# Optimization experiments

Measured on AMD Instinct MI355X. Metric: run time of the kernel, lower is better.

The kernel has to match this reference:

```python
import jax, jax.numpy as jnp
import numpy as np

B, LTMS, TTS, C_IN, F, H = 64, 16, 256, 128, 256, 256


def setup_inputs() -> dict:
    key = jax.random.key(0)
    ks = jax.random.split(key, 6)
    s = 0.05  # small init keeps relu-GRU numerically tame
    return {
        "x": jax.random.normal(ks[0], (B, LTMS * TTS, C_IN), dtype=jnp.float32),
        "conv_w": jax.random.normal(ks[1], (1, C_IN, F), dtype=jnp.float32) * s,
        "conv_b": jnp.zeros((F,), dtype=jnp.float32),
        "attn_w": jax.random.normal(ks[2], (TTS, TTS), dtype=jnp.float32) * s,
        "attn_b": jnp.zeros((TTS,), dtype=jnp.float32),
        "gru_w": jax.random.normal(ks[3], (F, 3 * H), dtype=jnp.float32) * s,
        "gru_u": jax.random.normal(ks[4], (H, 3 * H), dtype=jnp.float32) * s,
        "gru_b": jnp.zeros((2, 3 * H), dtype=jnp.float32),
    }


def _forward(x, conv_w, conv_b, attn_w, attn_b, gru_w, gru_u, gru_b):
    b = x.shape[0]
    # [B, LTMS*TTS, C] -> [B*LTMS, TTS, C]; segments are independent, so the
    # original per-segment Python loop vectorizes into the leading batch dim.
    xs = x.reshape(b * LTMS, TTS, C_IN)
    # Conv1D kernel_size=1 == pointwise GEMM, then ReLU (dropout=0 at inference)
    conv = jax.nn.relu(jnp.einsum('ntc,cf->ntf', xs, conv_w[0]) + conv_b)  # [N,T,F]
    # Attention: softmax(Dense) over time axis per filter, multiply back
    xt = conv.transpose(0, 2, 1)                                  # [N,F,T]
    probs = jax.nn.softmax(xt @ attn_w + attn_b, axis=-1)         # [N,F,T]
    x_att = conv * probs.transpose(0, 2, 1)                       # [N,T,F]
    # GRU (keras v2, reset_after=True), activation=relu, gate order z,r,h
    bi, br = gru_b[0], gru_b[1]
    gates_x = x_att @ gru_w + bi                                  # [N,T,3H]
    def step(h, gx):
        rec = h @ gru_u + br
        xz, xr, xh = jnp.split(gx, 3, axis=-1)
        rz, rr, rh = jnp.split(rec, 3, axis=-1)
        z = jax.nn.sigmoid(xz + rz)
        r = jax.nn.sigmoid(xr + rr)
        hh = jax.nn.relu(xh + r * rh)
        h_new = z * h + (1.0 - z) * hh
        return h_new, None
    h0 = jnp.zeros((b * LTMS, H), dtype=x.dtype)
    h_final, _ = jax.lax.scan(step, h0, gates_x.transpose(1, 0, 2))
    return h_final.reshape(b, LTMS, H)


def reference(x, conv_w, conv_b, attn_w, attn_b, gru_w, gru_u, gru_b):
    return _forward(x, conv_w, conv_b, attn_w, attn_b, gru_w, gru_u, gru_b)
```

## Files before the change

### kernel.cpp

```cpp
#include <hip/hip_runtime.h>
#include <stdint.h>

typedef unsigned short u16;
typedef __attribute__((ext_vector_type(8))) __bf16 bf16x8;
typedef __attribute__((ext_vector_type(4))) float f32x4;

#define TTS 256
#define NSEG 1024
#define TC 32

__device__ __forceinline__ u16 f2bf(float f) {
  union { float f; uint32_t u; } v; v.f = f;
  uint32_t r = v.u + 0x7fffu + ((v.u >> 16) & 1u);
  return (u16)(r >> 16);
}
__device__ __forceinline__ float bf2f(u16 h) {
  union { uint32_t u; float f; } v; v.u = ((uint32_t)h) << 16;
  return v.f;
}
__device__ __forceinline__ float sigm(float x) {
  return __builtin_amdgcn_rcpf(1.0f + __expf(-x));
}

__global__ void k_transp(const float* __restrict__ in, u16* __restrict__ out, int R, int C) {
  int i = blockIdx.x * blockDim.x + threadIdx.x;
  if (i < R * C) {
    int r = i / C, c = i % C;
    out[(size_t)c * R + r] = f2bf(in[i]);
  }
}

template <bool RELU, bool STORE_T, int AMODE>
__global__ __launch_bounds__(256) void k_gemm(
    const void* __restrict__ Av, const u16* __restrict__ Bt,
    const float* __restrict__ bias, u16* __restrict__ out, int K, int Nld, int t0) {
  __shared__ u16 ldsA[4096];
  __shared__ u16 ldsB[4096];
  const int tid  = threadIdx.x;
  const int w    = tid >> 6;
  const int lane = tid & 63;
  const int quad = lane >> 4;
  const int l16  = lane & 15;
  const int m0 = blockIdx.x * 128;
  const int n0 = blockIdx.y * 128;
  const int wm = w >> 1, wn = w & 1;
  const int srow = tid & 127, shalf = tid >> 7;

  f32x4 acc[4][4];
#pragma unroll
  for (int i = 0; i < 4; i++)
#pragma unroll
    for (int j = 0; j < 4; j++) acc[i][j] = f32x4{0.f, 0.f, 0.f, 0.f};

  for (int k0 = 0; k0 < K; k0 += 32) {
    ushort4 va[2][2]; bf16x8 vb[2];
#pragma unroll
    for (int q = 0; q < 2; q++) {
      int c = shalf * 2 + q;
      int kk = k0 + c * 8;
      if (AMODE == 0) {
        const float* Af = (const float*)Av;
        float4 f0 = *(const float4*)(Af + (size_t)(m0 + srow) * K + kk);
        float4 f1 = *(const float4*)(Af + (size_t)(m0 + srow) * K + kk + 4);
        va[q][0] = ushort4{f2bf(f0.x), f2bf(f0.y), f2bf(f0.z), f2bf(f0.w)};
        va[q][1] = ushort4{f2bf(f1.x), f2bf(f1.y), f2bf(f1.z), f2bf(f1.w)};
      } else {
        const u16* Ax = (const u16*)Av;
        int r = m0 + srow;
        const bf16x8 v = *(const bf16x8*)(Ax + (size_t)(r >> 5) * 65536 +
                          (size_t)(kk >> 6) * 16384 + (t0 + (r & 31)) * 64 + (kk & 63));
        va[q][0] = ((const ushort4*)&v)[0];
        va[q][1] = ((const ushort4*)&v)[1];
      }
      vb[q] = *(const bf16x8*)(Bt + (size_t)(n0 + srow) * K + kk);
    }
    __syncthreads();
#pragma unroll
    for (int q = 0; q < 2; q++) {
      int c = shalf * 2 + q;
      *(ushort4*)&ldsA[(c * 128 + srow) * 8]     = va[q][0];
      *(ushort4*)&ldsA[(c * 128 + srow) * 8 + 4] = va[q][1];
      *(bf16x8*)&ldsB[(c * 128 + srow) * 8] = vb[q];
    }
    __syncthreads();
    bf16x8 a[4], b[4];
#pragma unroll
    for (int i = 0; i < 4; i++)
      a[i] = *(const bf16x8*)&ldsA[(quad * 128 + wm * 64 + i * 16 + l16) * 8];
#pragma unroll
    for (int j = 0; j < 4; j++)
      b[j] = *(const bf16x8*)&ldsB[(quad * 128 + wn * 64 + j * 16 + l16) * 8];
#pragma unroll
    for (int i = 0; i < 4; i++)
#pragma unroll
      for (int j = 0; j < 4; j++)
        acc[i][j] = __builtin_amdgcn_mfma_f32_16x16x32_bf16(a[i], b[j], acc[i][j], 0, 0, 0);
  }

#pragma unroll
  for (int j = 0; j < 4; j++) {
    int col = n0 + wn * 64 + j * 16 + l16;
    float bv = bias[col];
#pragma unroll
    for (int i = 0; i < 4; i++) {
      int row0 = m0 + wm * 64 + i * 16 + quad * 4;
      if (STORE_T) {
        int nseg = row0 >> 8, tt0 = row0 & 255;
        ushort4 o;
        float v0 = acc[i][j][0] + bv, v1 = acc[i][j][1] + bv;
        float v2 = acc[i][j][2] + bv, v3 = acc[i][j][3] + bv;
        if (RELU) {
          v0 = fmaxf(v0, 0.f); v1 = fmaxf(v1, 0.f);
          v2 = fmaxf(v2, 0.f); v3 = fmaxf(v3, 0.f);
        }
        o.x = f2bf(v0); o.y = f2bf(v1); o.z = f2bf(v2); o.w = f2bf(v3);
        *(ushort4*)&out[(size_t)nseg * 65536 + (size_t)(col >> 6) * 16384 +
                        (col & 63) * 256 + tt0] = o;
      } else {
#pragma unroll
        for (int r = 0; r < 4; r++) {
          float v = acc[i][j][r] + bv;
          if (RELU) v = fmaxf(v, 0.f);
          out[(size_t)(row0 + r) * Nld + col] = f2bf(v);
        }
      }
    }
  }
}

__global__ __launch_bounds__(256) void k_attn(
    u16* xac,
    const u16* __restrict__ Wt,
    const float* __restrict__ attn_b) {
  __shared__ u16 ldsW[8192];
  __shared__ u16 ldsC[16384];
  __shared__ float redmax[4][64];
  __shared__ float redsum[4][64];
  const int tid  = threadIdx.x;
  const int w    = tid >> 6;
  const int lane = tid & 63;
  const int quad = lane >> 4;
  const int l16  = lane & 15;
  const int seg = blockIdx.x;
  const int c4  = blockIdx.y;
  u16* reg = xac + (size_t)seg * 65536 + (size_t)c4 * 16384;

  {
    const int f = tid & 63, g = tid >> 6;
#pragma unroll
    for (int u = 0; u < 8; u++) {
      int tch = g * 8 + u;
      *(bf16x8*)&ldsC[(tch * 64 + f) * 8] =
          *(const bf16x8*)(reg + (size_t)f * 256 + tch * 8);
    }
  }

  f32x4 acc[4][4];
#pragma unroll
  for (int i = 0; i < 4; i++)
#pragma unroll
    for (int j = 0; j < 4; j++) acc[i][j] = f32x4{0.f, 0.f, 0.f, 0.f};

  for (int s = 0; s < 8; s++) {
    int k0 = s * 32;
    bf16x8 vw[4];
#pragma unroll
    for (int c = 0; c < 4; c++)
      vw[c] = *(const bf16x8*)(Wt + (size_t)tid * 256 + k0 + c * 8);
    __syncthreads();
#pragma unroll
    for (int c = 0; c < 4; c++)
      *(bf16x8*)&ldsW[(c * 256 + tid) * 8] = vw[c];
    __syncthreads();
    bf16x8 a[4], b[4];
#pragma unroll
    for (int i = 0; i < 4; i++)
      a[i] = *(const bf16x8*)&ldsW[(quad * 256 + w * 64 + i * 16 + l16) * 8];
#pragma unroll
    for (int j = 0; j < 4; j++)
      b[j] = *(const bf16x8*)&ldsC[((s * 4 + quad) * 64 + j * 16 + l16) * 8];
#pragma unroll
    for (int i = 0; i < 4; i++)
#pragma unroll
      for (int j = 0; j < 4; j++)
        acc[i][j] = __builtin_amdgcn_mfma_f32_16x16x32_bf16(a[i], b[j], acc[i][j], 0, 0, 0);
  }

#pragma unroll
  for (int i = 0; i < 4; i++)
#pragma unroll
    for (int r = 0; r < 4; r++) {
      float ab = attn_b[w * 64 + i * 16 + quad * 4 + r];
#pragma unroll
      for (int j = 0; j < 4; j++) acc[i][j][r] += ab;
    }

  float lmax[4];
#pragma unroll
  for (int j = 0; j < 4; j++) {
    float m = -1e30f;
#pragma unroll
    for (int i = 0; i < 4; i++)
#pragma unroll
      for (int r = 0; r < 4; r++) m = fmaxf(m, acc[i][j][r]);
    m = fmaxf(m, __shfl_xor(m, 16));
    m = fmaxf(m, __shfl_xor(m, 32));
    lmax[j] = m;
  }
  __syncthreads();
  if (quad == 0) {
#pragma unroll
    for (int j = 0; j < 4; j++) redmax[w][j * 16 + l16] = lmax[j];
  }
  __syncthreads();
  float gmax[4];
#pragma unroll
  for (int j = 0; j < 4; j++) {
    int c = j * 16 + l16;
    gmax[j] = fmaxf(fmaxf(redmax[0][c], redmax[1][c]), fmaxf(redmax[2][c], redmax[3][c]));
  }
  float lsum[4];
#pragma unroll
  for (int j = 0; j < 4; j++) {
    float sacc = 0.f;
#pragma unroll
    for (int i = 0; i < 4; i++)
#pragma unroll
      for (int r = 0; r < 4; r++) {
        float e = __expf(acc[i][j][r] - gmax[j]);
        acc[i][j][r] = e;
        sacc += e;
      }
    sacc += __shfl_xor(sacc, 16);
    sacc += __shfl_xor(sacc, 32);
    lsum[j] = sacc;
  }
  if (quad == 0) {
#pragma unroll
    for (int j = 0; j < 4; j++) redsum[w][j * 16 + l16] = lsum[j];
  }
  __syncthreads();
  float rinv[4];
#pragma unroll
  for (int j = 0; j < 4; j++) {
    int c = j * 16 + l16;
    rinv[j] = 1.0f / (redsum[0][c] + redsum[1][c] + redsum[2][c] + redsum[3][c]);
  }

#pragma unroll
  for (int i = 0; i < 4; i++) {
#pragma unroll
    for (int r = 0; r < 4; r++) {
      int tp = w * 64 + i * 16 + quad * 4 + r;
#pragma unroll
      for (int j = 0; j < 4; j++) {
        int fl = j * 16 + l16;
        float cv = bf2f(ldsC[((tp >> 3) * 64 + fl) * 8 + (tp & 7)]);
        float xa = acc[i][j][r] * rinv[j] * cv;
        reg[(size_t)tp * 64 + fl] = f2bf(xa);
      }
    }
  }
}

__global__ __launch_bounds__(512, 2) void k_scanc(
    const u16* __restrict__ gc,
    const u16* __restrict__ Ut,
    const float* __restrict__ br,
    float* __restrict__ hio,
    int init) {
  __shared__ u16 uls[65536];
  __shared__ u16 hb[16 * 264];
  const int tid  = threadIdx.x;
  const int w    = tid >> 6;
  const int lane = tid & 63;
  const int quad = lane >> 4;
  const int l16  = lane & 15;
  const int n0 = blockIdx.x * 16;
  const int cg[2] = {w, 8 + w};

#pragma unroll
  for (int j = 0; j < 2; j++)
#pragma unroll
    for (int s = 0; s < 8; s++)
      *(bf16x8*)&uls[w * 8192 + (j * 8 + s) * 512 + lane * 8] =
          *(const bf16x8*)(Ut + (size_t)(j * 256 + cg[1] * 16 + l16) * 256 + s * 32 + quad * 8);

  bf16x8 ur0[3][8], urh1[8];
#pragma unroll
  for (int g = 0; g < 3; g++)
#pragma unroll
    for (int s = 0; s < 8; s++)
      ur0[g][s] = *(const bf16x8*)(Ut + (size_t)(g * 256 + cg[0] * 16 + l16) * 256 + s * 32 + quad * 8);
#pragma unroll
  for (int s = 0; s < 8; s++)
    urh1[s] = *(const bf16x8*)(Ut + (size_t)(512 + cg[1] * 16 + l16) * 256 + s * 32 + quad * 8);

  float brZ[2], brR[2], brH[2];
#pragma unroll
  for (int grp = 0; grp < 2; grp++) {
    int c = cg[grp] * 16 + l16;
    brZ[grp] = br[c]; brR[grp] = br[256 + c]; brH[grp] = br[512 + c];
  }

  float hreg[2][4];
#pragma unroll
  for (int grp = 0; grp < 2; grp++)
#pragma unroll
    for (int r = 0; r < 4; r++)
      hreg[grp][r] = init ? 0.f
                          : hio[(size_t)(n0 + quad * 4 + r) * 256 + cg[grp] * 16 + l16];
  {
    int sg = tid >> 5, c0 = (tid & 31) * 8;
    if (init) {
      *(ushort4*)&hb[sg * 264 + c0]     = ushort4{0, 0, 0, 0};
      *(ushort4*)&hb[sg * 264 + c0 + 4] = ushort4{0, 0, 0, 0};
    } else {
      const float* hp = hio + (size_t)(n0 + sg) * 256 + c0;
      float4 h0 = *(const float4*)(hp), h1 = *(const float4*)(hp + 4);
      *(ushort4*)&hb[sg * 264 + c0]     = ushort4{f2bf(h0.x), f2bf(h0.y), f2bf(h0.z), f2bf(h0.w)};
      *(ushort4*)&hb[sg * 264 + c0 + 4] = ushort4{f2bf(h1.x), f2bf(h1.y), f2bf(h1.z), f2bf(h1.w)};
    }
  }
  const u16* gseg[4];
#pragma unroll
  for (int r = 0; r < 4; r++)
    gseg[r] = gc + (size_t)(n0 + quad * 4 + r) * TC * 768;
  __syncthreads();

  for (int tt = 0; tt < TC; tt++) {
    float gg[2][3][4];
#pragma unroll
    for (int grp = 0; grp < 2; grp++)
#pragma unroll
      for (int g = 0; g < 3; g++)
#pragma unroll
        for (int r = 0; r < 4; r++)
          gg[grp][g][r] = bf2f(gseg[r][tt * 768 + g * 256 + cg[grp] * 16 + l16]);

    f32x4 acc[2][3];
#pragma unroll
    for (int grp = 0; grp < 2; grp++)
#pragma unroll
      for (int g = 0; g < 3; g++) acc[grp][g] = f32x4{0.f, 0.f, 0.f, 0.f};

#pragma unroll
    for (int s = 0; s < 8; s++) {
      bf16x8 ah = *(const bf16x8*)&hb[l16 * 264 + s * 32 + quad * 8];
#pragma unroll
      for (int g = 0; g < 3; g++)
        acc[0][g] = __builtin_amdgcn_mfma_f32_16x16x32_bf16(ah, ur0[g][s], acc[0][g], 0, 0, 0);
      bf16x8 uz = *(const bf16x8*)&uls[w * 8192 + s * 512 + lane * 8];
      bf16x8 urr = *(const bf16x8*)&uls[w * 8192 + (8 + s) * 512 + lane * 8];
      acc[1][0] = __builtin_amdgcn_mfma_f32_16x16x32_bf16(ah, uz,      acc[1][0], 0, 0, 0);
      acc[1][1] = __builtin_amdgcn_mfma_f32_16x16x32_bf16(ah, urr,     acc[1][1], 0, 0, 0);
      acc[1][2] = __builtin_amdgcn_mfma_f32_16x16x32_bf16(ah, urh1[s], acc[1][2], 0, 0, 0);
    }
    __syncthreads();

#pragma unroll
    for (int grp = 0; grp < 2; grp++)
#pragma unroll
      for (int r = 0; r < 4; r++) {
        float z  = sigm(acc[grp][0][r] + gg[grp][0][r] + brZ[grp]);
        float rg = sigm(acc[grp][1][r] + gg[grp][1][r] + brR[grp]);
        float hh = fmaxf(gg[grp][2][r] + rg * (acc[grp][2][r] + brH[grp]), 0.f);
        float hn = z * hreg[grp][r] + (1.0f - z) * hh;
        hreg[grp][r] = hn;
        hb[(quad * 4 + r) * 264 + cg[grp] * 16 + l16] = f2bf(hn);
      }
    __syncthreads();
  }

#pragma unroll
  for (int grp = 0; grp < 2; grp++)
#pragma unroll
    for (int r = 0; r < 4; r++)
      hio[(size_t)(n0 + quad * 4 + r) * 256 + cg[grp] * 16 + l16] = hreg[grp][r];
}

extern "C" void kernel_launch(void* const* d_in, const int* in_sizes, int n_in,
                              void* d_out, int out_size, void* d_ws, size_t ws_size,
                              hipStream_t stream) {
  (void)in_sizes; (void)n_in; (void)out_size;
  const float* x      = (const float*)d_in[0];
  const float* conv_w = (const float*)d_in[1];
  const float* conv_b = (const float*)d_in[2];
  const float* attn_w = (const float*)d_in[3];
  const float* attn_b = (const float*)d_in[4];
  const float* gru_w  = (const float*)d_in[5];
  const float* gru_u  = (const float*)d_in[6];
  const float* gru_b  = (const float*)d_in[7];

  const size_t NEEDED = 185532416;
  if (ws_size < NEEDED) return;
  char* ws = (char*)d_ws;
  u16* xac     = (u16*)(ws);
  u16* gatesC  = (u16*)(ws + 134217728);
  u16* conv_wT = (u16*)(ws + 184549376);
  u16* attn_wT = (u16*)(ws + 184614912);
  u16* gru_wT  = (u16*)(ws + 184745984);
  u16* gru_uT  = (u16*)(ws + 185139200);

  hipLaunchKernelGGL(k_transp, dim3(128), dim3(256), 0, stream, conv_w, conv_wT, 128, 256);
  hipLaunchKernelGGL(k_transp, dim3(256), dim3(256), 0, stream, attn_w, attn_wT, 256, 256);
  hipLaunchKernelGGL(k_transp, dim3(768), dim3(256), 0, stream, gru_w, gru_wT, 256, 768);
  hipLaunchKernelGGL(k_transp, dim3(768), dim3(256), 0, stream, gru_u, gru_uT, 256, 768);

  hipLaunchKernelGGL((k_gemm<true, true, 0>), dim3(2048, 2), dim3(256), 0, stream,
                     (const void*)x, conv_wT, conv_b, xac, 128, 0, 0);
  hipLaunchKernelGGL(k_attn, dim3(1024, 4), dim3(256), 0, stream,
                     xac, attn_wT, attn_b);
  for (int c = 0; c < 8; c++) {
    hipLaunchKernelGGL((k_gemm<false, false, 1>), dim3(256, 6), dim3(256), 0, stream,
                       (const void*)xac, gru_wT, gru_b, gatesC, 256, 768, c * TC);
    hipLaunchKernelGGL(k_scanc, dim3(64), dim3(512), 0, stream,
                       gatesC, gru_uT, gru_b + 768, (float*)d_out, c == 0 ? 1 : 0);
  }
}
```

Measured before the change: 1.262 ms.

## Widen GEMM tile to 128x256 with 512 threads and direct global-to-LDS loads

The GEMM kernel now uses 512-thread blocks covering a 128x256 output tile, so each A tile is loaded once per two former N-blocks. B tiles, and A tiles in the bf16 mode, are loaded with global_load_lds, which writes straight into LDS and skips the register staging. The launch grids are halved in N to match. LDS per block grows and occupancy constraints change, and the correctness of the direct LDS writes depends on the per-lane offset layout matching the intrinsic's addressing.

```diff
diff --git a/kernel.cpp b/kernel.cpp
--- a/kernel.cpp
+++ b/kernel.cpp
@@ -20,6 +20,11 @@
 }
 __device__ __forceinline__ float sigm(float x) {
   return __builtin_amdgcn_rcpf(1.0f + __expf(-x));
+}
+__device__ __forceinline__ void gl16(const void* g, void* l) {
+  __builtin_amdgcn_global_load_lds(
+      (const __attribute__((address_space(1))) unsigned int*)g,
+      (__attribute__((address_space(3))) unsigned int*)l, 16, 0, 0);
 }
 
 __global__ void k_transp(const float* __restrict__ in, u16* __restrict__ out, int R, int C) {
@@ -31,20 +36,20 @@
 }
 
 template <bool RELU, bool STORE_T, int AMODE>
-__global__ __launch_bounds__(256) void k_gemm(
+__global__ __launch_bounds__(512, 4) void k_gemm(
     const void* __restrict__ Av, const u16* __restrict__ Bt,
     const float* __restrict__ bias, u16* __restrict__ out, int K, int Nld, int t0) {
-  __shared__ u16 ldsA[4096];
-  __shared__ u16 ldsB[4096];
+  __shared__ __attribute__((aligned(16))) u16 ldsA[4096];
+  __shared__ __attribute__((aligned(16))) u16 ldsB[8192];
   const int tid  = threadIdx.x;
   const int w    = tid >> 6;
   const int lane = tid & 63;
   const int quad = lane >> 4;
   const int l16  = lane & 15;
   const int m0 = blockIdx.x * 128;
-  const int n0 = blockIdx.y * 128;
-  const int wm = w >> 1, wn = w & 1;
-  const int srow = tid & 127, shalf = tid >> 7;
+  const int n0 = blockIdx.y * 256;
+  const int wm = w >> 2, wn = w & 3;
+  const int arow = tid & 127, ac = tid >> 7;
 
   f32x4 acc[4][4];
 #pragma unroll
@@ -53,34 +58,32 @@
     for (int j = 0; j < 4; j++) acc[i][j] = f32x4{0.f, 0.f, 0.f, 0.f};
 
   for (int k0 = 0; k0 < K; k0 += 32) {
-    ushort4 va[2][2]; bf16x8 vb[2];
-#pragma unroll
-    for (int q = 0; q < 2; q++) {
-      int c = shalf * 2 + q;
-      int kk = k0 + c * 8;
-      if (AMODE == 0) {
-        const float* Af = (const float*)Av;
-        float4 f0 = *(const float4*)(Af + (size_t)(m0 + srow) * K + kk);
-        float4 f1 = *(const float4*)(Af + (size_t)(m0 + srow) * K + kk + 4);
-        va[q][0] = ushort4{f2bf(f0.x), f2bf(f0.y), f2bf(f0.z), f2bf(f0.w)};
-        va[q][1] = ushort4{f2bf(f1.x), f2bf(f1.y), f2bf(f1.z), f2bf(f1.w)};
-      } else {
-        const u16* Ax = (const u16*)Av;
-        int r = m0 + srow;
-        const bf16x8 v = *(const bf16x8*)(Ax + (size_t)(r >> 5) * 65536 +
-                          (size_t)(kk >> 6) * 16384 + (t0 + (r & 31)) * 64 + (kk & 63));
-        va[q][0] = ((const ushort4*)&v)[0];
-        va[q][1] = ((const ushort4*)&v)[1];
-      }
-      vb[q] = *(const bf16x8*)(Bt + (size_t)(n0 + srow) * K + kk);
-    }
-    __syncthreads();
-#pragma unroll
-    for (int q = 0; q < 2; q++) {
-      int c = shalf * 2 + q;
-      *(ushort4*)&ldsA[(c * 128 + srow) * 8]     = va[q][0];
-      *(ushort4*)&ldsA[(c * 128 + srow) * 8 + 4] = va[q][1];
-      *(bf16x8*)&ldsB[(c * 128 + srow) * 8] = vb[q];
+    ushort4 va0, va1;
+    if (AMODE == 0) {
+      const float* Af = (const float*)Av;
+      const float* p = Af + (size_t)(m0 + arow) * K + k0 + ac * 8;
+      float4 f0 = *(const float4*)p;
+      float4 f1 = *(const float4*)(p + 4);
+      va0 = ushort4{f2bf(f0.x), f2bf(f0.y), f2bf(f0.z), f2bf(f0.w)};
+      va1 = ushort4{f2bf(f1.x), f2bf(f1.y), f2bf(f1.z), f2bf(f1.w)};
+    }
+    __syncthreads();
+    if (AMODE == 0) {
+      *(ushort4*)&ldsA[tid * 8]     = va0;
+      *(ushort4*)&ldsA[tid * 8 + 4] = va1;
+    } else {
+      const u16* Ax = (const u16*)Av;
+      int r = m0 + arow;
+      int kk = k0 + ac * 8;
+      gl16(Ax + (size_t)(r >> 5) * 65536 + (size_t)(kk >> 6) * 16384 +
+               (t0 + (r & 31)) * 64 + (kk & 63),
+           &ldsA[tid * 8]);
+    }
+#pragma unroll
+    for (int i = 0; i < 2; i++) {
+      int idx = i * 512 + tid;
+      int brow = idx & 255, bc = idx >> 8;
+      gl16(Bt + (size_t)(n0 + brow) * K + k0 + bc * 8, &ldsB[idx * 8]);
     }
     __syncthreads();
     bf16x8 a[4], b[4];
@@ -89,7 +92,7 @@
       a[i] = *(const bf16x8*)&ldsA[(quad * 128 + wm * 64 + i * 16 + l16) * 8];
 #pragma unroll
     for (int j = 0; j < 4; j++)
-      b[j] = *(const bf16x8*)&ldsB[(quad * 128 + wn * 64 + j * 16 + l16) * 8];
+      b[j] = *(const bf16x8*)&ldsB[(quad * 256 + wn * 64 + j * 16 + l16) * 8];
 #pragma unroll
     for (int i = 0; i < 4; i++)
 #pragma unroll
@@ -407,12 +410,12 @@
   hipLaunchKernelGGL(k_transp, dim3(768), dim3(256), 0, stream, gru_w, gru_wT, 256, 768);
   hipLaunchKernelGGL(k_transp, dim3(768), dim3(256), 0, stream, gru_u, gru_uT, 256, 768);
 
-  hipLaunchKernelGGL((k_gemm<true, true, 0>), dim3(2048, 2), dim3(256), 0, stream,
+  hipLaunchKernelGGL((k_gemm<true, true, 0>), dim3(2048, 1), dim3(512), 0, stream,
                      (const void*)x, conv_wT, conv_b, xac, 128, 0, 0);
   hipLaunchKernelGGL(k_attn, dim3(1024, 4), dim3(256), 0, stream,
                      xac, attn_wT, attn_b);
   for (int c = 0; c < 8; c++) {
-    hipLaunchKernelGGL((k_gemm<false, false, 1>), dim3(256, 6), dim3(256), 0, stream,
+    hipLaunchKernelGGL((k_gemm<false, false, 1>), dim3(256, 3), dim3(512), 0, stream,
                        (const void*)xac, gru_wT, gru_b, gatesC, 256, 768, c * TC);
     hipLaunchKernelGGL(k_scanc, dim3(64), dim3(512), 0, stream,
                        gatesC, gru_uT, gru_b + 768, (float*)d_out, c == 0 ? 1 : 0);
```

After: 1.243 ms. Within noise of the previous version (-1.5%).
